# Kernel tuning notes

Hardware: AMD Instinct MI355X
Metric: run time of the kernel (lower is better)

The kernel has to match this reference:

```python
import jax, jax.numpy as jnp
import numpy as np

B, C_IN, C_OUT, K, N = 8, 16, 16, 4, 524288


def setup_inputs() -> dict:
    key = jax.random.key(0)
    k1, k2, k3 = jax.random.split(key, 3)
    inp = jax.random.normal(k1, (B, C_IN, N), dtype=jnp.float32)
    # reset_parameters: uniform(-stdv, stdv) with stdv = 1/sqrt(in_channels * kernel_size)
    stdv = 1.0 / np.sqrt(C_IN * K)
    weight = jax.random.uniform(k2, (C_OUT, K, C_IN), dtype=jnp.float32,
                                minval=-stdv, maxval=stdv)
    attention_score = jax.random.normal(k3, (B, K, N), dtype=jnp.float32)
    return {"input": inp, "weight": weight, "attention_score": attention_score}


def reference(input, weight, attention_score):
    # out[b,o,n] = sum_{k,c} input[b,c,n] * weight[o,k,c] * attention_score[b,k,n]
    # Loop over the small fixed kernel_size K to avoid a [B,K,C,N] intermediate.
    out = jnp.zeros((input.shape[0], weight.shape[0], input.shape[2]), dtype=input.dtype)
    for k in range(weight.shape[1]):
        # weight per-tap gemm on score-weighted input: [O,C] x [B,C,N] -> [B,O,N]
        out = out + jnp.einsum('oc,bcn->bon', weight[:, k, :],
                               input * attention_score[:, k:k + 1, :])
    return out
```

## Files before the change

### kernel.cpp

```cpp
#include <hip/hip_runtime.h>
#include <hip/hip_bf16.h>


constexpr int B     = 8;
constexpr int C_IN  = 16;
constexpr int C_OUT = 16;
constexpr int KK    = 4;
constexpr long NN   = 524288;
constexpr int W     = 256;
constexpr int S     = 8;
constexpr int BPB   = (int)(NN / (W * S));
constexpr int GRID  = B * BPB;

typedef short bf16x8 __attribute__((ext_vector_type(8)));
typedef float f32x4  __attribute__((ext_vector_type(4)));

__device__ inline short f2bf(float f) {
    return __builtin_bit_cast(short, __float2bfloat16(f));
}

__device__ inline void gll16(const float* gsrc, float* ldst) {
    __builtin_amdgcn_global_load_lds(
        (const __attribute__((address_space(1))) unsigned int*)gsrc,
        (__attribute__((address_space(3))) unsigned int*)ldst,
        16, 0, 0);
}

__global__ __launch_bounds__(256, 3) void
TransformConv1d_39264591020709_kernel(const float* __restrict__ in,
                                      const float* __restrict__ w,
                                      const float* __restrict__ sc,
                                      float* __restrict__ out) {
    __shared__ float lds[3][C_IN][W];

    const int tid  = threadIdx.x;
    const int lane = tid & 63;
    const int wid  = tid >> 6;
    const int g    = lane >> 4;
    const int col  = lane & 15;

    const int  bi = blockIdx.x;
    const int  b  = bi >> 8;
    const long n0 = (long)(bi & (BPB - 1)) * (W * S);

    const int ktap = g >> 1;
    const int c0   = (g & 1) * 8;

    bf16x8 w0, w1;
#pragma unroll
    for (int i = 0; i < 8; ++i) {
        w0[i] = f2bf(w[(col * KK + ktap    ) * C_IN + c0 + i]);
        w1[i] = f2bf(w[(col * KK + ktap + 2) * C_IN + c0 + i]);
    }

    const float* inb  = in  + (long)b * C_IN  * NN;
    const float* scb  = sc  + (long)b * KK    * NN;
    float*       outb = out + (long)b * C_OUT * NN;

    auto STAGE = [&](int s) {
        const long noff = n0 + (long)s * W;
#pragma unroll
        for (int j = 0; j < 4; ++j) {
            const int r = wid * 4 + j;
            gll16(inb + (long)r * NN + noff + lane * 4, &lds[s % 3][r][0]);
        }
    };

    auto SCORES = [&](int s, float (&a0)[4], float (&a1)[4]) {
        const long nb = n0 + (long)s * W;
#pragma unroll
        for (int u = 0; u < 4; ++u) {
            const int nc = (wid * 4 + u) * 16 + col;
            a0[u] = scb[(long)ktap       * NN + nb + nc];
            a1[u] = scb[(long)(ktap + 2) * NN + nb + nc];
        }
    };

    STAGE(0);
    STAGE(1);
    float a0c[4], a1c[4];
    SCORES(0, a0c, a1c);
    asm volatile("s_waitcnt vmcnt(12)" ::: "memory");
    __builtin_amdgcn_sched_barrier(0);
    __builtin_amdgcn_s_barrier();
    __builtin_amdgcn_sched_barrier(0);

#pragma unroll
    for (int s = 0; s < S; ++s) {
        const long nb = n0 + (long)s * W;
        float (*X)[W] = lds[s % 3];

        float a0n[4], a1n[4];
        if (s + 1 < S) SCORES(s + 1, a0n, a1n);
        __builtin_amdgcn_sched_barrier(0);
        if (s + 2 < S) STAGE(s + 2);
        __builtin_amdgcn_sched_barrier(0);

#pragma unroll
        for (int u = 0; u < 4; ++u) {
            const int nt = (wid * 4 + u) * 16;
            float xv[8];
#pragma unroll
            for (int i = 0; i < 8; ++i) xv[i] = X[c0 + i][nt + col];
            bf16x8 z0, z1;
#pragma unroll
            for (int i = 0; i < 8; ++i) {
                z0[i] = f2bf(a0c[u] * xv[i]);
                z1[i] = f2bf(a1c[u] * xv[i]);
            }
            f32x4 acc = {0.f, 0.f, 0.f, 0.f};
            acc = __builtin_amdgcn_mfma_f32_16x16x32_bf16(w0, z0, acc, 0, 0, 0);
            acc = __builtin_amdgcn_mfma_f32_16x16x32_bf16(w1, z1, acc, 0, 0, 0);
#pragma unroll
            for (int r = 0; r < 4; ++r)
                X[g * 4 + r][nt + col] = acc[r];
        }
        __builtin_amdgcn_sched_barrier(0);

#pragma unroll
        for (int q = 0; q < 4; ++q) {
            const int row = q * 4 + (lane >> 4);
            const int cq  = wid * 64 + (lane & 15) * 4;
            f32x4 v = *(const f32x4*)&X[row][cq];
            __builtin_nontemporal_store(v,
                (f32x4*)(outb + (long)row * NN + nb + cq));
        }

        if (s + 1 < S) {
            if (s + 2 < S)
                asm volatile("s_waitcnt vmcnt(20)" ::: "memory");
            else
                asm volatile("s_waitcnt vmcnt(16)" ::: "memory");
            __builtin_amdgcn_sched_barrier(0);
            __builtin_amdgcn_s_barrier();
            __builtin_amdgcn_sched_barrier(0);
        }

#pragma unroll
        for (int u = 0; u < 4; ++u) { a0c[u] = a0n[u]; a1c[u] = a1n[u]; }
    }
}

extern "C" void kernel_launch(void* const* d_in, const int* in_sizes, int n_in,
                              void* d_out, int out_size, void* d_ws, size_t ws_size,
                              hipStream_t stream) {
    const float* in = (const float*)d_in[0];
    const float* w  = (const float*)d_in[1];
    const float* sc = (const float*)d_in[2];
    float* out = (float*)d_out;

    TransformConv1d_39264591020709_kernel<<<GRID, 256, 0, stream>>>(in, w, sc, out);
}
```

Before: 116.9 us.

## Make LDS tiles wave-private to drop block barriers and shrink staging buffers

After: 120.9 us. +3.4%, slower.

```diff
diff --git a/kernel.cpp b/kernel.cpp
--- a/kernel.cpp
+++ b/kernel.cpp
@@ -7,9 +7,8 @@
 constexpr int C_OUT = 16;
 constexpr int KK    = 4;
 constexpr long NN   = 524288;
-constexpr int W     = 256;
 constexpr int S     = 8;
-constexpr int BPB   = (int)(NN / (W * S));
+constexpr int BPB   = (int)(NN / (256 * S));
 constexpr int GRID  = B * BPB;
 
 typedef short bf16x8 __attribute__((ext_vector_type(8)));
@@ -26,22 +25,24 @@
         16, 0, 0);
 }
 
-__global__ __launch_bounds__(256, 3) void
+__global__ __launch_bounds__(256, 5) void
 TransformConv1d_39264591020709_kernel(const float* __restrict__ in,
                                       const float* __restrict__ w,
                                       const float* __restrict__ sc,
                                       float* __restrict__ out) {
-    __shared__ float lds[3][C_IN][W];
+    __shared__ float lds[2][4][C_IN][64];
 
     const int tid  = threadIdx.x;
     const int lane = tid & 63;
     const int wid  = tid >> 6;
     const int g    = lane >> 4;
     const int col  = lane & 15;
+    const int lr   = lane >> 4;
+    const int lc4  = (lane & 15) * 4;
 
     const int  bi = blockIdx.x;
     const int  b  = bi >> 8;
-    const long n0 = (long)(bi & (BPB - 1)) * (W * S);
+    const long n0 = (long)(bi & (BPB - 1)) * (256 * S);
 
     const int ktap = g >> 1;
     const int c0   = (g & 1) * 8;
@@ -58,50 +59,48 @@
     float*       outb = out + (long)b * C_OUT * NN;
 
     auto STAGE = [&](int s) {
-        const long noff = n0 + (long)s * W;
+        const long nw = n0 + (long)s * 256 + wid * 64;
 #pragma unroll
-        for (int j = 0; j < 4; ++j) {
-            const int r = wid * 4 + j;
-            gll16(inb + (long)r * NN + noff + lane * 4, &lds[s % 3][r][0]);
+        for (int j = 0; j < 4; ++j)
+            gll16(inb + (long)(4 * j + lr) * NN + nw + lc4,
+                  &lds[s & 1][wid][4 * j][0]);
+    };
+
+    auto SCORES = [&](int s, float (&a0)[4], float (&a1)[4]) {
+        const long nw = n0 + (long)s * 256 + wid * 64;
+#pragma unroll
+        for (int u = 0; u < 4; ++u) {
+            a0[u] = scb[(long)ktap       * NN + nw + u * 16 + col];
+            a1[u] = scb[(long)(ktap + 2) * NN + nw + u * 16 + col];
         }
     };
 
-    auto SCORES = [&](int s, float (&a0)[4], float (&a1)[4]) {
-        const long nb = n0 + (long)s * W;
-#pragma unroll
-        for (int u = 0; u < 4; ++u) {
-            const int nc = (wid * 4 + u) * 16 + col;
-            a0[u] = scb[(long)ktap       * NN + nb + nc];
-            a1[u] = scb[(long)(ktap + 2) * NN + nb + nc];
-        }
-    };
-
-    STAGE(0);
-    STAGE(1);
     float a0c[4], a1c[4];
     SCORES(0, a0c, a1c);
-    asm volatile("s_waitcnt vmcnt(12)" ::: "memory");
-    __builtin_amdgcn_sched_barrier(0);
-    __builtin_amdgcn_s_barrier();
-    __builtin_amdgcn_sched_barrier(0);
+    STAGE(0);
 
 #pragma unroll
     for (int s = 0; s < S; ++s) {
-        const long nb = n0 + (long)s * W;
-        float (*X)[W] = lds[s % 3];
+        const long nw = n0 + (long)s * 256 + wid * 64;
+        float (*X)[64] = lds[s & 1][wid];
 
         float a0n[4], a1n[4];
-        if (s + 1 < S) SCORES(s + 1, a0n, a1n);
+        if (s + 1 < S) {
+            SCORES(s + 1, a0n, a1n);
+            STAGE(s + 1);
+        }
         __builtin_amdgcn_sched_barrier(0);
-        if (s + 2 < S) STAGE(s + 2);
+
+        if (s == 0)          asm volatile("s_waitcnt vmcnt(12)" ::: "memory");
+        else if (s + 1 < S)  asm volatile("s_waitcnt vmcnt(16)" ::: "memory");
+        else                 asm volatile("s_waitcnt vmcnt(4)"  ::: "memory");
         __builtin_amdgcn_sched_barrier(0);
 
 #pragma unroll
         for (int u = 0; u < 4; ++u) {
-            const int nt = (wid * 4 + u) * 16;
             float xv[8];
 #pragma unroll
-            for (int i = 0; i < 8; ++i) xv[i] = X[c0 + i][nt + col];
+            for (int i = 0; i < 8; ++i) xv[i] = X[c0 + i][u * 16 + col];
             bf16x8 z0, z1;
 #pragma unroll
             for (int i = 0; i < 8; ++i) {
@@ -113,27 +112,15 @@
             acc = __builtin_amdgcn_mfma_f32_16x16x32_bf16(w1, z1, acc, 0, 0, 0);
 #pragma unroll
             for (int r = 0; r < 4; ++r)
-                X[g * 4 + r][nt + col] = acc[r];
+                X[g * 4 + r][u * 16 + col] = acc[r];
         }
         __builtin_amdgcn_sched_barrier(0);
 
 #pragma unroll
         for (int q = 0; q < 4; ++q) {
-            const int row = q * 4 + (lane >> 4);
-            const int cq  = wid * 64 + (lane & 15) * 4;
-            f32x4 v = *(const f32x4*)&X[row][cq];
-            __builtin_nontemporal_store(v,
-                (f32x4*)(outb + (long)row * NN + nb + cq));
-        }
-
-        if (s + 1 < S) {
-            if (s + 2 < S)
-                asm volatile("s_waitcnt vmcnt(20)" ::: "memory");
-            else
-                asm volatile("s_waitcnt vmcnt(16)" ::: "memory");
-            __builtin_amdgcn_sched_barrier(0);
-            __builtin_amdgcn_s_barrier();
-            __builtin_amdgcn_sched_barrier(0);
+            const int row = q * 4 + lr;
+            f32x4 v = *(const f32x4*)&X[row][lc4];
+            __builtin_nontemporal_store(v, (f32x4*)(outb + (long)row * NN + nw + lc4));
         }
 
 #pragma unroll
```
